# Kernel tuning notes

Hardware: AMD Instinct MI355X
Metric: run time of the kernel (lower is better)

Reference implementation:

```python
import jax, jax.numpy as jnp
import numpy as np

R, S, H, B = 50000, 8, 128, 4096

def setup_inputs() -> dict:
    key = jax.random.key(0)
    ks = jax.random.split(key, 8)
    return {
        "memory": jax.random.normal(ks[0], (R, S, H), dtype=jnp.float32) * 0.02,
        "o_emb_w": jax.random.normal(ks[1], (H,), dtype=jnp.float32),
        "o_emb_r": jax.random.normal(ks[2], (B, H), dtype=jnp.float32),
        "attn_W": jax.random.normal(ks[3], (H, H), dtype=jnp.float32) * (1.0 / np.sqrt(H)),
        "sim_w": jax.random.normal(ks[4], (2 * H, 1), dtype=jnp.float32) * 0.05,
        "sim_b": jax.random.normal(ks[5], (1,), dtype=jnp.float32) * 0.05,
        "forget_w": jax.random.normal(ks[6], (2 * H, 1), dtype=jnp.float32) * 0.05,
        "o_rg": 12345,
        "d_rg": jax.random.randint(ks[7], (B,), 0, R, dtype=jnp.int32),
    }

def reference(memory, o_emb_w, o_emb_r, attn_W, sim_w, sim_b, forget_w, o_rg, d_rg):
    h = memory.shape[-1]
    # --- write (state='w'): gather one region, sigmoid forget gate, scatter update ---
    sel = memory[o_rg]                                   # [S, H]
    o_ext = jnp.broadcast_to(o_emb_w, sel.shape)         # [S, H]
    # forget_linear(cat([o_emb, mem])) with no bias
    gate = jax.nn.sigmoid(o_ext @ forget_w[:h] + sel @ forget_w[h:])  # [S, 1]
    new_slot = sel * (1.0 - gate) + o_ext * gate
    new_mem = memory.at[o_rg].set(new_slot)              # equivalent to memory*(1-pad)+o_emb*pad
    # --- read (state='r'): gather per-batch region, concat-MLP attention over slots ---
    km = new_mem[d_rg]                                   # [B, S, H]
    q = o_emb_r @ attn_W                                 # [B, H]
    kv = km @ attn_W                                     # [B, S, H] (key == value input, same projection)
    # sim_mlp = Linear(2H,1)+ReLU applied to cat([q, k]), then softmax over slot dim
    logits = jax.nn.relu((q @ sim_w[:h])[:, None, :] + kv @ sim_w[h:] + sim_b)  # [B, S, 1]
    score = jax.nn.softmax(logits, axis=-2)              # softmax over slots
    mem_out = jnp.sum(score * kv, axis=-2)               # [B, H]
    return mem_out
```

## Files before the change

kernel.cpp:

```cpp
#include <hip/hip_runtime.h>
#include <math.h>

#define H  128
#define S  8
#define BB 8

__device__ __forceinline__ float wave_sum(float v) {
    #pragma unroll
    for (int off = 32; off; off >>= 1) v += __shfl_xor(v, off, 64);
    return v;
}

__global__ __launch_bounds__(512) void fused_kernel(
        const float* __restrict__ memory,
        const float* __restrict__ o_emb_w,
        const float* __restrict__ o_emb_r,
        const float* __restrict__ attn_W,
        const float* __restrict__ sim_w,
        const float* __restrict__ sim_b,
        const float* __restrict__ forget_w,
        const int*   __restrict__ o_rg_p,
        const int*   __restrict__ d_rg,
        float* __restrict__ out) {
    __shared__ float v1s[H], v2s[H];
    __shared__ float wm_lds[BB][H];

    const int u  = threadIdx.x;
    const int wv = u >> 6;
    const int L  = u & 63;
    const int c  = L & 31;
    const int hi = L >> 5;
    const int b  = blockIdx.x * BB + wv;

    const int o_rg = o_rg_p[0];
    const int r    = d_rg[b];

    const float4* src4 = (const float4*)(memory + (size_t)r * (S * H));
    float4 rows[4];
    #pragma unroll
    for (int j = 0; j < 4; ++j) rows[j] = src4[j * 64 + L];
    const float2 oe = ((const float2*)o_emb_r)[(size_t)b * (H / 2) + L];

    if (u < 256) {
        const int row = u & 127;
        const float4* wr = (const float4*)(attn_W + row * H);
        const float4* sv = (const float4*)(sim_w + (u >> 7) * H);
        float a = 0.f;
        #pragma unroll 8
        for (int j = 0; j < 32; ++j) {
            float4 w = wr[j], x = sv[j];
            a += w.x * x.x + w.y * x.y + w.z * x.z + w.w * x.w;
        }
        if (u < 128) v1s[row] = a; else v2s[row] = a;
    }
    __syncthreads();

    if (r == o_rg) {
        const float4 ow4 = ((const float4*)o_emb_w)[c];
        const float4 f24 = ((const float4*)(forget_w + H))[c];
        const float2 ow2 = ((const float2*)o_emb_w)[L];
        const float2 f12 = ((const float2*)forget_w)[L];
        const float base = wave_sum(ow2.x * f12.x + ow2.y * f12.y);
        #pragma unroll
        for (int j = 0; j < 4; ++j) {
            float v = rows[j].x * f24.x + rows[j].y * f24.y
                    + rows[j].z * f24.z + rows[j].w * f24.w;
            #pragma unroll
            for (int off = 1; off <= 16; off <<= 1) v += __shfl_xor(v, off, 64);
            float g = 1.f / (1.f + expf(-(base + v)));
            rows[j].x = rows[j].x * (1.f - g) + ow4.x * g;
            rows[j].y = rows[j].y * (1.f - g) + ow4.y * g;
            rows[j].z = rows[j].z * (1.f - g) + ow4.z * g;
            rows[j].w = rows[j].w * (1.f - g) + ow4.w * g;
        }
    }

    const float2 vv1 = ((const float2*)v1s)[L];
    const float  qs  = wave_sum(oe.x * vv1.x + oe.y * vv1.y);
    const float4 vv2 = ((const float4*)v2s)[c];

    float d2own[4], d2oth[4];
    #pragma unroll
    for (int j = 0; j < 4; ++j) {
        float v = rows[j].x * vv2.x + rows[j].y * vv2.y
                + rows[j].z * vv2.z + rows[j].w * vv2.w;
        #pragma unroll
        for (int off = 1; off <= 16; off <<= 1) v += __shfl_xor(v, off, 64);
        d2own[j] = v;
        d2oth[j] = __shfl_xor(v, 32, 64);
    }

    const float sb = sim_b[0];
    float lown[4], loth[4], m = -INFINITY;
    #pragma unroll
    for (int j = 0; j < 4; ++j) {
        lown[j] = fmaxf(qs + d2own[j] + sb, 0.f);
        loth[j] = fmaxf(qs + d2oth[j] + sb, 0.f);
        m = fmaxf(m, fmaxf(lown[j], loth[j]));
    }
    float pown[4], psum = 0.f;
    #pragma unroll
    for (int j = 0; j < 4; ++j) {
        pown[j] = expf(lown[j] - m);
        psum += pown[j] + expf(loth[j] - m);
    }
    const float inv = 1.f / psum;

    float4 wm = {0.f, 0.f, 0.f, 0.f};
    #pragma unroll
    for (int j = 0; j < 4; ++j) {
        float ps = pown[j] * inv;
        wm.x += ps * rows[j].x;
        wm.y += ps * rows[j].y;
        wm.z += ps * rows[j].z;
        wm.w += ps * rows[j].w;
    }
    wm.x += __shfl_xor(wm.x, 32, 64);
    wm.y += __shfl_xor(wm.y, 32, 64);
    wm.z += __shfl_xor(wm.z, 32, 64);
    wm.w += __shfl_xor(wm.w, 32, 64);
    if (hi == 0) ((float4*)wm_lds[wv])[c] = wm;
    __syncthreads();

    const float4* W4 = (const float4*)attn_W;
    const float* wmrow = wm_lds[wv];
    float4 acc = {0.f, 0.f, 0.f, 0.f};
    #pragma unroll 8
    for (int j = 0; j < 64; ++j) {
        int i = hi * 64 + j;
        float4 w = W4[i * (H / 4) + c];
        float  x = wmrow[i];
        acc.x += x * w.x;
        acc.y += x * w.y;
        acc.z += x * w.z;
        acc.w += x * w.w;
    }
    acc.x += __shfl_xor(acc.x, 32, 64);
    acc.y += __shfl_xor(acc.y, 32, 64);
    acc.z += __shfl_xor(acc.z, 32, 64);
    acc.w += __shfl_xor(acc.w, 32, 64);
    if (hi == 0) ((float4*)out)[(size_t)b * (H / 4) + c] = acc;
}

extern "C" void kernel_launch(void* const* d_in, const int* in_sizes, int n_in,
                              void* d_out, int out_size, void* d_ws, size_t ws_size,
                              hipStream_t stream) {
    const float* memory   = (const float*)d_in[0];
    const float* o_emb_w  = (const float*)d_in[1];
    const float* o_emb_r  = (const float*)d_in[2];
    const float* attn_W   = (const float*)d_in[3];
    const float* sim_w    = (const float*)d_in[4];
    const float* sim_b    = (const float*)d_in[5];
    const float* forget_w = (const float*)d_in[6];
    const int*   o_rg     = (const int*)d_in[7];
    const int*   d_rg     = (const int*)d_in[8];
    float* out = (float*)d_out;

    const int B = in_sizes[8];

    fused_kernel<<<B / BB, 512, 0, stream>>>(
        memory, o_emb_w, o_emb_r, attn_W, sim_w, sim_b, forget_w, o_rg, d_rg, out);
}
```

Baseline: 265.1 us.

## Hold attn_W slices in registers and split final projection across waves via LDS reduction

The final wm @ attn_W projection is restructured. Each of the 16 half-waves now keeps an 8-row slice of attn_W in registers and computes partial products for all 8 batch rows in the block. The partials are then reduced through a shared-memory union buffer instead of each wave streaming the whole 64KB matrix. The sim_w projection also fuses the two dot products into one pass over 128 threads, and launch bounds request 4 blocks per CU. In exchange this adds LDS traffic, two extra barriers, a 16-way reduction step and more register pressure.

```diff
diff --git a/kernel.cpp b/kernel.cpp
--- a/kernel.cpp
+++ b/kernel.cpp
@@ -11,7 +11,7 @@
     return v;
 }
 
-__global__ __launch_bounds__(512) void fused_kernel(
+__global__ __launch_bounds__(512, 4) void fused_kernel(
         const float* __restrict__ memory,
         const float* __restrict__ o_emb_w,
         const float* __restrict__ o_emb_r,
@@ -22,8 +22,10 @@
         const int*   __restrict__ o_rg_p,
         const int*   __restrict__ d_rg,
         float* __restrict__ out) {
-    __shared__ float v1s[H], v2s[H];
-    __shared__ float wm_lds[BB][H];
+    __shared__ union SM {
+        struct { float v1s[H]; float v2s[H]; float wm[BB][H]; } a;
+        float4 part[2 * BB][BB][H / 4];
+    } sm;
 
     const int u  = threadIdx.x;
     const int wv = u >> 6;
@@ -41,17 +43,25 @@
     for (int j = 0; j < 4; ++j) rows[j] = src4[j * 64 + L];
     const float2 oe = ((const float2*)o_emb_r)[(size_t)b * (H / 2) + L];
 
-    if (u < 256) {
-        const int row = u & 127;
-        const float4* wr = (const float4*)(attn_W + row * H);
-        const float4* sv = (const float4*)(sim_w + (u >> 7) * H);
-        float a = 0.f;
+    const int i0 = wv * 16 + hi * 8;
+    const float4* W4 = (const float4*)attn_W;
+    float4 Wreg[8];
+    #pragma unroll
+    for (int k = 0; k < 8; ++k) Wreg[k] = W4[(i0 + k) * (H / 4) + c];
+
+    if (u < H) {
+        const float4* wr = W4 + u * (H / 4);
+        const float4* s1 = (const float4*)sim_w;
+        const float4* s2 = (const float4*)(sim_w + H);
+        float a1 = 0.f, a2 = 0.f;
         #pragma unroll 8
         for (int j = 0; j < 32; ++j) {
-            float4 w = wr[j], x = sv[j];
-            a += w.x * x.x + w.y * x.y + w.z * x.z + w.w * x.w;
+            float4 w = wr[j], x1 = s1[j], x2 = s2[j];
+            a1 += w.x * x1.x + w.y * x1.y + w.z * x1.z + w.w * x1.w;
+            a2 += w.x * x2.x + w.y * x2.y + w.z * x2.z + w.w * x2.w;
         }
-        if (u < 128) v1s[row] = a; else v2s[row] = a;
+        sm.a.v1s[u] = a1;
+        sm.a.v2s[u] = a2;
     }
     __syncthreads();
 
@@ -75,9 +85,9 @@
         }
     }
 
-    const float2 vv1 = ((const float2*)v1s)[L];
+    const float2 vv1 = ((const float2*)sm.a.v1s)[L];
     const float  qs  = wave_sum(oe.x * vv1.x + oe.y * vv1.y);
-    const float4 vv2 = ((const float4*)v2s)[c];
+    const float4 vv2 = ((const float4*)sm.a.v2s)[c];
 
     float d2own[4], d2oth[4];
     #pragma unroll
@@ -119,27 +129,42 @@
     wm.y += __shfl_xor(wm.y, 32, 64);
     wm.z += __shfl_xor(wm.z, 32, 64);
     wm.w += __shfl_xor(wm.w, 32, 64);
-    if (hi == 0) ((float4*)wm_lds[wv])[c] = wm;
+    if (hi == 0) ((float4*)sm.a.wm[wv])[c] = wm;
     __syncthreads();
 
-    const float4* W4 = (const float4*)attn_W;
-    const float* wmrow = wm_lds[wv];
-    float4 acc = {0.f, 0.f, 0.f, 0.f};
-    #pragma unroll 8
-    for (int j = 0; j < 64; ++j) {
-        int i = hi * 64 + j;
-        float4 w = W4[i * (H / 4) + c];
-        float  x = wmrow[i];
-        acc.x += x * w.x;
-        acc.y += x * w.y;
-        acc.z += x * w.z;
-        acc.w += x * w.w;
+    float4 acc[BB];
+    const int q0 = i0 >> 2;
+    #pragma unroll
+    for (int bb = 0; bb < BB; ++bb) {
+        const float4 m0 = ((const float4*)sm.a.wm[bb])[q0];
+        const float4 m1 = ((const float4*)sm.a.wm[bb])[q0 + 1];
+        float4 a;
+        a.x = m0.x * Wreg[0].x + m0.y * Wreg[1].x + m0.z * Wreg[2].x + m0.w * Wreg[3].x
+            + m1.x * Wreg[4].x + m1.y * Wreg[5].x + m1.z * Wreg[6].x + m1.w * Wreg[7].x;
+        a.y = m0.x * Wreg[0].y + m0.y * Wreg[1].y + m0.z * Wreg[2].y + m0.w * Wreg[3].y
+            + m1.x * Wreg[4].y + m1.y * Wreg[5].y + m1.z * Wreg[6].y + m1.w * Wreg[7].y;
+        a.z = m0.x * Wreg[0].z + m0.y * Wreg[1].z + m0.z * Wreg[2].z + m0.w * Wreg[3].z
+            + m1.x * Wreg[4].z + m1.y * Wreg[5].z + m1.z * Wreg[6].z + m1.w * Wreg[7].z;
+        a.w = m0.x * Wreg[0].w + m0.y * Wreg[1].w + m0.z * Wreg[2].w + m0.w * Wreg[3].w
+            + m1.x * Wreg[4].w + m1.y * Wreg[5].w + m1.z * Wreg[6].w + m1.w * Wreg[7].w;
+        acc[bb] = a;
     }
-    acc.x += __shfl_xor(acc.x, 32, 64);
-    acc.y += __shfl_xor(acc.y, 32, 64);
-    acc.z += __shfl_xor(acc.z, 32, 64);
-    acc.w += __shfl_xor(acc.w, 32, 64);
-    if (hi == 0) ((float4*)out)[(size_t)b * (H / 4) + c] = acc;
+    __syncthreads();
+
+    #pragma unroll
+    for (int bb = 0; bb < BB; ++bb) sm.part[wv * 2 + hi][bb][c] = acc[bb];
+    __syncthreads();
+
+    if (u < 256) {
+        const int bb = u >> 5, cc = u & 31;
+        float4 s0 = sm.part[0][bb][cc];
+        #pragma unroll
+        for (int k = 1; k < 16; ++k) {
+            const float4 p = sm.part[k][bb][cc];
+            s0.x += p.x; s0.y += p.y; s0.z += p.z; s0.w += p.w;
+        }
+        ((float4*)out)[(size_t)(blockIdx.x * BB + bb) * (H / 4) + cc] = s0;
+    }
 }
 
 extern "C" void kernel_launch(void* const* d_in, const int* in_sizes, int n_in,
```

Result: faster. 254.8 us (-3.9%).
